# Kernel optimization log

Hardware: AMD Instinct MI355X
Metric: run time of the kernel (lower is better)

The kernel has to match this reference:

```python
import jax, jax.numpy as jnp
import numpy as np
from jax import lax

NUM_SPLIT = 16
DCT = 7
# top16 frequency indices (first 16 of the top lists)
MAPPER_X = np.array([0, 0, 6, 0, 0, 1, 1, 4, 5, 1, 3, 0, 0, 0, 3, 2], dtype=np.int32)
MAPPER_Y = np.array([0, 1, 0, 5, 2, 0, 2, 0, 0, 6, 0, 4, 6, 3, 5, 2], dtype=np.int32)


def _dct_table():
    pos = np.arange(DCT)
    freq = np.arange(DCT)[:, None]
    d = np.cos(np.pi * freq * (pos + 0.5) / DCT) / np.sqrt(DCT)
    d[1:] *= np.sqrt(2.0)
    return d.astype(np.float32)  # (7, 7): [freq, pos]


def _gconv(x, w, b, groups):
    y = lax.conv_general_dilated(x, w, (2, 2), 'VALID',
                                 dimension_numbers=('NCHW', 'OIHW', 'NCHW'),
                                 feature_group_count=groups)
    return y + b[None, :, None, None]


def setup_inputs() -> dict:
    key = jax.random.key(0)
    ks = jax.random.split(key, 7)
    n, c, h, w = 32, 512, 56, 56
    r = 16
    return {
        'x': jax.random.normal(ks[0], (n, c, h, w), jnp.float32),
        'conv1_w': jax.random.normal(ks[1], (NUM_SPLIT, c // NUM_SPLIT, 3, 3), jnp.float32) * 0.05,
        'conv1_b': jax.random.normal(ks[2], (NUM_SPLIT,), jnp.float32) * 0.05,
        'conv2_w': jax.random.normal(ks[3], (NUM_SPLIT, 1, 3, 3), jnp.float32) * 0.3,
        'conv2_b': jax.random.normal(ks[4], (NUM_SPLIT,), jnp.float32) * 0.3,
        'w1': jax.random.normal(ks[5], (c // r, c), jnp.float32) * 0.05,
        'w2': jax.random.normal(ks[6], (c, c // r), jnp.float32) * 0.2,
    }


def reference(x, conv1_w, conv1_b, conv2_w, conv2_b, w1, w2):
    n, c, h, w = x.shape
    c_part = c // NUM_SPLIT
    D = jnp.asarray(_dct_table(), x.dtype)
    mx = jnp.asarray(MAPPER_X)
    my = jnp.asarray(MAPPER_Y)

    # adaptive_avg_pool2d to 7x7 (h,w divisible by 7 -> exact block mean)
    xp = x.reshape(n, c, DCT, h // DCT, DCT, w // DCT).mean(axis=(3, 5))

    # filters_predicted: grouped conv 7x7 -> 3x3 -> 1x1
    a1 = jax.nn.hard_sigmoid(_gconv(xp, conv1_w, conv1_b, NUM_SPLIT))
    v = _gconv(a1, conv2_w, conv2_b, NUM_SPLIT).reshape(n, NUM_SPLIT)
    # adaptive_avg_pool1d(1 -> 16) repeats v; matmul with ones(16,1) sums -> v * 16
    pred = jnp.clip(v * NUM_SPLIT, 0.0, NUM_SPLIT - 1.1)

    left = pred.astype(jnp.int32)   # (n, 16)
    frac = pred - left
    right = left + 1

    def dct_weights(idx):  # idx (n,16) -> per-split 7x7 DCT filters (n,16,7,7)
        fx = D[mx[idx]]  # (n,16,7)
        fy = D[my[idx]]
        return fx[..., :, None] * fy[..., None, :]

    xp_s = xp.reshape(n, NUM_SPLIT, c_part, DCT, DCT)
    res_l = jnp.einsum('nskhw,nshw->nsk', xp_s, dct_weights(left)) * (1.0 - frac)[:, :, None]
    res_r = jnp.einsum('nskhw,nshw->nsk', xp_s, dct_weights(right)) * frac[:, :, None]
    s = (res_l + res_r).reshape(n, c)

    hmid = jax.nn.hard_sigmoid(s @ w1.T)
    cw = jax.nn.sigmoid(hmid @ w2.T)  # (n, c)
    return x * cw[:, :, None, None]
```

## Files before the change

kernel.cpp:

```cpp
#include <hip/hip_runtime.h>

#define N_   32
#define C_   512
#define H_   56
#define W_   56
#define S_   16
#define CP_  32
#define HW_  (H_*W_)
#define TOT_ ((size_t)N_*C_*HW_)

typedef float f32x4 __attribute__((ext_vector_type(4)));

__constant__ int d_mx[16] = {0,0,6,0,0,1,1,4,5,1,3,0,0,0,3,2};
__constant__ int d_my[16] = {0,1,0,5,2,0,2,0,0,6,0,4,6,3,5,2};

__global__ void __launch_bounds__(256) pool_kernel(const float* __restrict__ x,
                                                   float* __restrict__ xp) {
    __shared__ float tile[HW_];
    __shared__ float part[49 * 4];
    int plane = blockIdx.x;
    int t = threadIdx.x;
    const float4* src = reinterpret_cast<const float4*>(x + (size_t)plane * HW_);
    for (int i = t; i < HW_ / 4; i += 256)
        *reinterpret_cast<float4*>(&tile[i * 4]) = src[i];
    __syncthreads();
    if (t < 196) {
        int bin = t >> 2, q = t & 3;
        int oi = bin / 7, oj = bin % 7;
        const float* rp = &tile[(oi * 8 + q * 2) * W_ + oj * 8];
        float s = 0.f;
#pragma unroll
        for (int rr = 0; rr < 2; ++rr)
#pragma unroll
            for (int cc = 0; cc < 8; ++cc) s += rp[rr * W_ + cc];
        part[t] = s;
    }
    __syncthreads();
    if (t < 49) {
        float s = part[t * 4] + part[t * 4 + 1] + part[t * 4 + 2] + part[t * 4 + 3];
        xp[(size_t)plane * 49 + t] = s * (1.0f / 64.0f);
    }
}

__global__ void __launch_bounds__(256, 4) hs_kernel(
        const float* __restrict__ x,
        const float* __restrict__ xp,
        const float* __restrict__ c1w, const float* __restrict__ c1b,
        const float* __restrict__ c2w, const float* __restrict__ c2b,
        const float* __restrict__ w1,  const float* __restrict__ w2,
        float* __restrict__ out) {
    __shared__ float sD[49];
    __shared__ float a1[S_ * 9];
    __shared__ float wcomb[S_ * 49];
    __shared__ float svec[C_];
    __shared__ float hpart[256];
    __shared__ float hmid[32];
    __shared__ float cwv[8];
    __shared__ float sfrac[S_];
    __shared__ int   sleft[S_];

    const int bid = blockIdx.x, t = threadIdx.x;
    const int n = bid >> 6;
    const int r = bid & 63;
    const float* xpn = xp + (size_t)n * C_ * 49;

    if (t >= 192 && t < 241) {
        int u = t - 192, f = u / 7, p = u - f * 7;
        float v = cosf(3.14159265358979323846f * f * (p + 0.5f) / 7.0f) * 0.3779644730092272f;
        if (f >= 1) v *= 1.4142135623730951f;
        sD[u] = v;
    }
    if (t < S_ * 9) {
        int s = t / 9, o = t - s * 9, oi = o / 3, oj = o - oi * 3;
        float acc = c1b[s];
        const float* xb = xpn + s * CP_ * 49;
        const float* wb = c1w + s * CP_ * 9;
        for (int ic = 0; ic < CP_; ++ic) {
#pragma unroll
            for (int ki = 0; ki < 3; ++ki)
#pragma unroll
                for (int kj = 0; kj < 3; ++kj)
                    acc += xb[ic * 49 + (oi * 2 + ki) * 7 + (oj * 2 + kj)]
                         * wb[ic * 9 + ki * 3 + kj];
        }
        a1[t] = fminf(fmaxf(acc + 3.f, 0.f), 6.f) * (1.f / 6.f);
    }
    __syncthreads();

    if (t < S_) {
        float acc = c2b[t];
#pragma unroll
        for (int k = 0; k < 9; ++k) acc += a1[t * 9 + k] * c2w[t * 9 + k];
        float pred = fminf(fmaxf(acc * 16.f, 0.f), 14.9f);
        int l = (int)pred;
        sleft[t] = l;
        sfrac[t] = pred - (float)l;
    }
    __syncthreads();

    for (int i = t; i < S_ * 49; i += 256) {
        int s = i / 49, p = i - s * 49, hh = p / 7, ww = p - hh * 7;
        int l = sleft[s], rr = l + 1;
        float fr = sfrac[s];
        wcomb[i] = (1.f - fr) * sD[d_mx[l] * 7 + hh] * sD[d_my[l] * 7 + ww]
                 +        fr  * sD[d_mx[rr] * 7 + hh] * sD[d_my[rr] * 7 + ww];
    }
    __syncthreads();

#pragma unroll
    for (int q = 0; q < 2; ++q) {
        int ch = t + q * 256;
        const float* xb = xpn + ch * 49;
        const float* wb = &wcomb[(ch >> 5) * 49];
        float acc = 0.f;
#pragma unroll
        for (int p = 0; p < 49; ++p) acc += xb[p] * wb[p];
        svec[ch] = acc;
    }
    __syncthreads();

    {
        int o = t >> 3, g = t & 7;
        const f32x4* wv = reinterpret_cast<const f32x4*>(w1 + o * C_ + g * 64);
        const f32x4* sv = reinterpret_cast<const f32x4*>(&svec[g * 64]);
        float acc = 0.f;
#pragma unroll
        for (int j = 0; j < 16; ++j) {
            f32x4 a = sv[j], b = wv[j];
            acc += a.x * b.x + a.y * b.y + a.z * b.z + a.w * b.w;
        }
        hpart[t] = acc;
    }
    __syncthreads();
    if (t < 32) {
        float acc = 0.f;
#pragma unroll
        for (int g = 0; g < 8; ++g) acc += hpart[t * 8 + g];
        hmid[t] = fminf(fmaxf(acc + 3.f, 0.f), 6.f) * (1.f / 6.f);
    }
    __syncthreads();

    if (t < 8) {
        int c = r * 8 + t;
        const f32x4* hv = reinterpret_cast<const f32x4*>(hmid);
        const f32x4* wr = reinterpret_cast<const f32x4*>(w2 + c * 32);
        float acc = 0.f;
#pragma unroll
        for (int j = 0; j < 8; ++j) {
            f32x4 h = hv[j], b = wr[j];
            acc += h.x * b.x + h.y * b.y + h.z * b.z + h.w * b.w;
        }
        cwv[t] = 1.f / (1.f + expf(-acc));
    }
    __syncthreads();

#pragma unroll 1
    for (int k = 0; k < 8; ++k) {
        const int plane = n * C_ + r * 8 + k;
        const float wsc = cwv[k];
        const f32x4* src = reinterpret_cast<const f32x4*>(x + (size_t)plane * HW_);
        f32x4* dst = reinterpret_cast<f32x4*>(out + (size_t)plane * HW_);
        f32x4 u0 = src[t];
        f32x4 u1 = src[t + 256];
        f32x4 u2 = src[t + 512];
        f32x4 u3;
        if (t < 16) u3 = src[t + 768];
        u0 *= wsc; u1 *= wsc; u2 *= wsc;
        __builtin_nontemporal_store(u0, dst + t);
        __builtin_nontemporal_store(u1, dst + t + 256);
        __builtin_nontemporal_store(u2, dst + t + 512);
        if (t < 16) {
            u3 *= wsc;
            __builtin_nontemporal_store(u3, dst + t + 768);
        }
    }
}

extern "C" void kernel_launch(void* const* d_in, const int* in_sizes, int n_in,
                              void* d_out, int out_size, void* d_ws, size_t ws_size,
                              hipStream_t stream) {
    const float* x   = (const float*)d_in[0];
    const float* c1w = (const float*)d_in[1];
    const float* c1b = (const float*)d_in[2];
    const float* c2w = (const float*)d_in[3];
    const float* c2b = (const float*)d_in[4];
    const float* w1  = (const float*)d_in[5];
    const float* w2  = (const float*)d_in[6];
    float* out = (float*)d_out;

    float* xp = (float*)d_ws;

    pool_kernel<<<N_ * C_, 256, 0, stream>>>(x, xp);
    hs_kernel<<<N_ * S_ * 4, 256, 0, stream>>>(x, xp, c1w, c1b, c2w, c2b, w1, w2, out);
}
```

Before: 430.9 us.

## Split head computation into one block per batch and separate scale kernel

The previous fused kernel recomputed the whole per-sample head (conv, DCT, both FCs) in each of 64 blocks per sample, then scaled 8 planes each. The head now runs once per sample in a 32-block kernel that writes channel weights to workspace, and a plane-per-block scale kernel applies them. The pool kernel also drops the full-plane shared-memory staging: it reduces float4 groups in registers and sums 14-wide rows from a smaller shared buffer. This removes redundant head work at the cost of an extra launch and a serial low-parallelism head kernel between pooling and scaling.

```diff
diff --git a/kernel.cpp b/kernel.cpp
--- a/kernel.cpp
+++ b/kernel.cpp
@@ -16,52 +16,46 @@
 
 __global__ void __launch_bounds__(256) pool_kernel(const float* __restrict__ x,
                                                    float* __restrict__ xp) {
-    __shared__ float tile[HW_];
-    __shared__ float part[49 * 4];
+    __shared__ float part[784];
     int plane = blockIdx.x;
     int t = threadIdx.x;
-    const float4* src = reinterpret_cast<const float4*>(x + (size_t)plane * HW_);
-    for (int i = t; i < HW_ / 4; i += 256)
-        *reinterpret_cast<float4*>(&tile[i * 4]) = src[i];
+    const f32x4* src = reinterpret_cast<const f32x4*>(x + (size_t)plane * HW_);
+    f32x4 u0 = src[t];
+    f32x4 u1 = src[t + 256];
+    f32x4 u2 = src[t + 512];
+    f32x4 u3;
+    if (t < 16) u3 = src[t + 768];
+    part[t]       = u0.x + u0.y + u0.z + u0.w;
+    part[t + 256] = u1.x + u1.y + u1.z + u1.w;
+    part[t + 512] = u2.x + u2.y + u2.z + u2.w;
+    if (t < 16) part[t + 768] = u3.x + u3.y + u3.z + u3.w;
     __syncthreads();
-    if (t < 196) {
-        int bin = t >> 2, q = t & 3;
-        int oi = bin / 7, oj = bin % 7;
-        const float* rp = &tile[(oi * 8 + q * 2) * W_ + oj * 8];
+    if (t < 49) {
+        int rb = t / 7, cb = t - rb * 7;
+        const float* p = &part[rb * 8 * 14 + cb * 2];
         float s = 0.f;
 #pragma unroll
-        for (int rr = 0; rr < 2; ++rr)
-#pragma unroll
-            for (int cc = 0; cc < 8; ++cc) s += rp[rr * W_ + cc];
-        part[t] = s;
-    }
-    __syncthreads();
-    if (t < 49) {
-        float s = part[t * 4] + part[t * 4 + 1] + part[t * 4 + 2] + part[t * 4 + 3];
+        for (int r = 0; r < 8; ++r) s += p[r * 14] + p[r * 14 + 1];
         xp[(size_t)plane * 49 + t] = s * (1.0f / 64.0f);
     }
 }
 
-__global__ void __launch_bounds__(256, 4) hs_kernel(
-        const float* __restrict__ x,
+__global__ void __launch_bounds__(256) head_kernel(
         const float* __restrict__ xp,
         const float* __restrict__ c1w, const float* __restrict__ c1b,
         const float* __restrict__ c2w, const float* __restrict__ c2b,
         const float* __restrict__ w1,  const float* __restrict__ w2,
-        float* __restrict__ out) {
+        float* __restrict__ cwout) {
     __shared__ float sD[49];
     __shared__ float a1[S_ * 9];
     __shared__ float wcomb[S_ * 49];
     __shared__ float svec[C_];
     __shared__ float hpart[256];
     __shared__ float hmid[32];
-    __shared__ float cwv[8];
     __shared__ float sfrac[S_];
     __shared__ int   sleft[S_];
 
-    const int bid = blockIdx.x, t = threadIdx.x;
-    const int n = bid >> 6;
-    const int r = bid & 63;
+    const int n = blockIdx.x, t = threadIdx.x;
     const float* xpn = xp + (size_t)n * C_ * 49;
 
     if (t >= 192 && t < 241) {
@@ -100,10 +94,10 @@
 
     for (int i = t; i < S_ * 49; i += 256) {
         int s = i / 49, p = i - s * 49, hh = p / 7, ww = p - hh * 7;
-        int l = sleft[s], rr = l + 1;
+        int l = sleft[s], r = l + 1;
         float fr = sfrac[s];
         wcomb[i] = (1.f - fr) * sD[d_mx[l] * 7 + hh] * sD[d_my[l] * 7 + ww]
-                 +        fr  * sD[d_mx[rr] * 7 + hh] * sD[d_my[rr] * 7 + ww];
+                 +        fr  * sD[d_mx[r] * 7 + hh] * sD[d_my[r] * 7 + ww];
     }
     __syncthreads();
 
@@ -140,39 +134,46 @@
     }
     __syncthreads();
 
-    if (t < 8) {
-        int c = r * 8 + t;
+#pragma unroll
+    for (int q = 0; q < 2; ++q) {
+        int ch = t + q * 256;
+        const f32x4* wr = reinterpret_cast<const f32x4*>(w2 + ch * 32);
         const f32x4* hv = reinterpret_cast<const f32x4*>(hmid);
-        const f32x4* wr = reinterpret_cast<const f32x4*>(w2 + c * 32);
         float acc = 0.f;
 #pragma unroll
         for (int j = 0; j < 8; ++j) {
             f32x4 h = hv[j], b = wr[j];
             acc += h.x * b.x + h.y * b.y + h.z * b.z + h.w * b.w;
         }
-        cwv[t] = 1.f / (1.f + expf(-acc));
+        cwout[n * C_ + ch] = 1.f / (1.f + expf(-acc));
     }
-    __syncthreads();
+}
 
-#pragma unroll 1
-    for (int k = 0; k < 8; ++k) {
-        const int plane = n * C_ + r * 8 + k;
-        const float wsc = cwv[k];
-        const f32x4* src = reinterpret_cast<const f32x4*>(x + (size_t)plane * HW_);
-        f32x4* dst = reinterpret_cast<f32x4*>(out + (size_t)plane * HW_);
-        f32x4 u0 = src[t];
-        f32x4 u1 = src[t + 256];
-        f32x4 u2 = src[t + 512];
-        f32x4 u3;
-        if (t < 16) u3 = src[t + 768];
-        u0 *= wsc; u1 *= wsc; u2 *= wsc;
-        __builtin_nontemporal_store(u0, dst + t);
-        __builtin_nontemporal_store(u1, dst + t + 256);
-        __builtin_nontemporal_store(u2, dst + t + 512);
-        if (t < 16) {
-            u3 *= wsc;
-            __builtin_nontemporal_store(u3, dst + t + 768);
-        }
+__global__ void __launch_bounds__(256) scale_kernel(const float* __restrict__ x,
+                                                    const float* __restrict__ cw,
+                                                    float* __restrict__ out) {
+    int plane = blockIdx.x;
+    int t = threadIdx.x;
+    float wsc = cw[plane];
+    const f32x4* src = reinterpret_cast<const f32x4*>(x + (size_t)plane * HW_);
+    f32x4* dst = reinterpret_cast<f32x4*>(out + (size_t)plane * HW_);
+
+    f32x4 u0 = src[t];
+    f32x4 u1 = src[t + 256];
+    f32x4 u2 = src[t + 512];
+    f32x4 u3;
+    if (t < 16) u3 = src[t + 768];
+
+    u0 *= wsc;
+    u1 *= wsc;
+    u2 *= wsc;
+
+    __builtin_nontemporal_store(u0, dst + t);
+    __builtin_nontemporal_store(u1, dst + t + 256);
+    __builtin_nontemporal_store(u2, dst + t + 512);
+    if (t < 16) {
+        u3 *= wsc;
+        __builtin_nontemporal_store(u3, dst + t + 768);
     }
 }
 
@@ -188,8 +189,10 @@
     const float* w2  = (const float*)d_in[6];
     float* out = (float*)d_out;
 
-    float* xp = (float*)d_ws;
+    float* xp    = (float*)d_ws;
+    float* cwbuf = xp + (size_t)N_ * C_ * 49;
 
     pool_kernel<<<N_ * C_, 256, 0, stream>>>(x, xp);
-    hs_kernel<<<N_ * S_ * 4, 256, 0, stream>>>(x, xp, c1w, c1b, c2w, c2b, w1, w2, out);
+    head_kernel<<<N_, 256, 0, stream>>>(xp, c1w, c1b, c2w, c2b, w1, w2, cwbuf);
+    scale_kernel<<<N_ * C_, 256, 0, stream>>>(x, cwbuf, out);
 }
```

Result: faster. 393.2 us, median of 2 (-8.7%).
